# Performance work log

Measured on AMD Instinct MI355X. Metric: run time of the kernel, lower is better.

## Reference

```python
import jax, jax.numpy as jnp
import numpy as np

N, E, T = 4096, 49152, 262144
H, EMB, AIN, EB, TB = 256, 64, 92, 80, 40
NBLK = 12  # 4 alignn * 2 EGGC + 4 gcn


def _ln(x, s, b):
    mu = jnp.mean(x, -1, keepdims=True)
    v = jnp.mean((x - mu) ** 2, -1, keepdims=True)
    return (x - mu) * jax.lax.rsqrt(v + 1e-5) * s + b


def _mlp(x, W, b, s, bi):
    # Linear -> LayerNorm -> SiLU (MLPLayer)
    return jax.nn.silu(_ln(x @ W + b, s, bi))


def _rbf(x, vmin, vmax, bins):
    centers = jnp.linspace(vmin, vmax, bins)
    gamma = 1.0 / ((vmax - vmin) / (bins - 1))
    return jnp.exp(-gamma * (x[:, None] - centers) ** 2)


def _eggc(x, e, src, dst, W, b, ln_s, ln_b, n_nodes):
    # W: [5,H,H] = src_gate, dst_gate, edge_gate, src_update, dst_update
    m = (x @ W[0] + b[0])[src] + (x @ W[1] + b[1])[dst] + (e @ W[2] + b[2])
    sigma = jax.nn.sigmoid(m)
    sum_sh = jax.ops.segment_sum((x @ W[4] + b[4])[src] * sigma, dst, num_segments=n_nodes)
    sum_s = jax.ops.segment_sum(sigma, dst, num_segments=n_nodes)
    h = sum_sh / (sum_s + 1e-6)
    x_new = jax.nn.silu(_ln(x @ W[3] + b[3] + h, ln_s[0], ln_b[0]))
    e_new = jax.nn.silu(_ln(m, ln_s[1], ln_b[1]))
    return x + x_new, e + e_new  # residual=True


def setup_inputs() -> dict:
    key = jax.random.key(0)
    ks = jax.random.split(key, 16)
    s = 0.05
    return {
        "atom_features": jax.random.normal(ks[0], (N, AIN), jnp.float32),
        "r": jax.random.normal(ks[1], (E, 3), jnp.float32),
        "src": jax.random.randint(ks[2], (E,), 0, N),
        "dst": jax.random.randint(ks[3], (E,), 0, N),
        "lsrc": jax.random.randint(ks[4], (T,), 0, E),
        "ldst": jax.random.randint(ks[5], (T,), 0, E),
        "atom_W": s * jax.random.normal(ks[6], (AIN, H), jnp.float32),
        "atom_b": jnp.zeros((H,), jnp.float32),
        "atom_ln_s": jnp.ones((H,), jnp.float32),
        "atom_ln_b": jnp.zeros((H,), jnp.float32),
        "edge_W1": s * jax.random.normal(ks[7], (EB, EMB), jnp.float32),
        "edge_b1": jnp.zeros((EMB,), jnp.float32),
        "edge_ln1_s": jnp.ones((EMB,), jnp.float32),
        "edge_ln1_b": jnp.zeros((EMB,), jnp.float32),
        "edge_W2": s * jax.random.normal(ks[8], (EMB, H), jnp.float32),
        "edge_b2": jnp.zeros((H,), jnp.float32),
        "edge_ln2_s": jnp.ones((H,), jnp.float32),
        "edge_ln2_b": jnp.zeros((H,), jnp.float32),
        "ang_W1": s * jax.random.normal(ks[9], (TB, EMB), jnp.float32),
        "ang_b1": jnp.zeros((EMB,), jnp.float32),
        "ang_ln1_s": jnp.ones((EMB,), jnp.float32),
        "ang_ln1_b": jnp.zeros((EMB,), jnp.float32),
        "ang_W2": s * jax.random.normal(ks[10], (EMB, H), jnp.float32),
        "ang_b2": jnp.zeros((H,), jnp.float32),
        "ang_ln2_s": jnp.ones((H,), jnp.float32),
        "ang_ln2_b": jnp.zeros((H,), jnp.float32),
        "eggc_W": s * jax.random.normal(ks[11], (NBLK, 5, H, H), jnp.float32),
        "eggc_b": jnp.zeros((NBLK, 5, H), jnp.float32),
        "eggc_ln_s": jnp.ones((NBLK, 2, H), jnp.float32),
        "eggc_ln_b": jnp.zeros((NBLK, 2, H), jnp.float32),
        "fc_W": s * jax.random.normal(ks[12], (H, 1), jnp.float32),
        "fc_b": jnp.zeros((1,), jnp.float32),
    }


def reference(atom_features, r, src, dst, lsrc, ldst,
              atom_W, atom_b, atom_ln_s, atom_ln_b,
              edge_W1, edge_b1, edge_ln1_s, edge_ln1_b,
              edge_W2, edge_b2, edge_ln2_s, edge_ln2_b,
              ang_W1, ang_b1, ang_ln1_s, ang_ln1_b,
              ang_W2, ang_b2, ang_ln2_s, ang_ln2_b,
              eggc_W, eggc_b, eggc_ln_s, eggc_ln_b, fc_W, fc_b):
    # line-graph bond cosines: cos(-r_i, r_j) for each bond pair
    r1, r2 = -r[lsrc], r[ldst]
    cos = jnp.sum(r1 * r2, -1) / (jnp.linalg.norm(r1, axis=-1) * jnp.linalg.norm(r2, axis=-1))
    cos = jnp.clip(cos, -1.0, 1.0)
    z = _mlp(_mlp(_rbf(cos, -1.0, 1.0, TB), ang_W1, ang_b1, ang_ln1_s, ang_ln1_b),
             ang_W2, ang_b2, ang_ln2_s, ang_ln2_b)
    x = _mlp(atom_features, atom_W, atom_b, atom_ln_s, atom_ln_b)
    bondlength = jnp.linalg.norm(r, axis=1)
    y = _mlp(_mlp(_rbf(bondlength, 0.0, 8.0, EB), edge_W1, edge_b1, edge_ln1_s, edge_ln1_b),
             edge_W2, edge_b2, edge_ln2_s, edge_ln2_b)
    for i in range(4):  # alignn layers: crystal graph then line graph
        x, m = _eggc(x, y, src, dst, eggc_W[2 * i], eggc_b[2 * i], eggc_ln_s[2 * i], eggc_ln_b[2 * i], N)
        y, z = _eggc(m, z, lsrc, ldst, eggc_W[2 * i + 1], eggc_b[2 * i + 1], eggc_ln_s[2 * i + 1], eggc_ln_b[2 * i + 1], E)
    for i in range(4):  # gcn layers
        j = 8 + i
        x, y = _eggc(x, y, src, dst, eggc_W[j], eggc_b[j], eggc_ln_s[j], eggc_ln_b[j], N)
    atomwise_energy = x @ fc_W + fc_b  # [N,1]
    total_energy = jnp.mean(atomwise_energy)  # AvgPooling (eV/atom), single graph
    return total_energy, atomwise_energy
```

## Files before the change

### kernel.cpp

```cpp
#include <hip/hip_runtime.h>


typedef unsigned short bfu;
typedef __attribute__((ext_vector_type(8))) short short8;
typedef __attribute__((ext_vector_type(4))) float floatx4;

#define CHN 4096
#define CHCAP 24576
#define HH 65536

__device__ __forceinline__ float bf2f(bfu u) {
  union { unsigned u; float f; } x; x.u = ((unsigned)u) << 16; return x.f;
}
__device__ __forceinline__ bfu f2bf(float f) {
  union { float f; unsigned u; } x; x.f = f;
  unsigned r = x.u + 0x7FFFu + ((x.u >> 16) & 1u);
  return (bfu)(r >> 16);
}
__device__ __forceinline__ float fsig(float x) {
  return __builtin_amdgcn_rcpf(1.f + __expf(-x));
}
__device__ __forceinline__ float fsilu(float x) { return x * fsig(x); }

__device__ __forceinline__ void load_lds16(const bfu* g, bfu* l) {
  __builtin_amdgcn_global_load_lds(
      (const __attribute__((address_space(1))) void*)g,
      (__attribute__((address_space(3))) void*)l, 16, 0, 0);
}

struct f8 { float v[8]; };
__device__ __forceinline__ f8 ld8(const bfu* p) {
  short8 u = *(const short8*)(const void*)p;
  f8 r;
#pragma unroll
  for (int i = 0; i < 8; ++i) r.v[i] = bf2f((bfu)u[i]);
  return r;
}
__device__ __forceinline__ void st8(bfu* p, f8 x) {
  short8 u;
#pragma unroll
  for (int i = 0; i < 8; ++i) u[i] = (short)f2bf(x.v[i]);
  *(short8*)(void*)p = u;
}
__device__ __forceinline__ f8 add8(f8 a, f8 b) {
  f8 r;
#pragma unroll
  for (int i = 0; i < 8; ++i) r.v[i] = a.v[i] + b.v[i];
  return r;
}
__device__ __forceinline__ f8 sig8(f8 m) {
  f8 r;
#pragma unroll
  for (int i = 0; i < 8; ++i) r.v[i] = fsig(m.v[i]);
  return r;
}
__device__ __forceinline__ void wstats32(const f8& x, float& mean, float& rstd) {
  float s = 0.f, q = 0.f;
#pragma unroll
  for (int i = 0; i < 8; ++i) { s += x.v[i]; q += x.v[i] * x.v[i]; }
#pragma unroll
  for (int m = 1; m < 32; m <<= 1) { s += __shfl_xor(s, m); q += __shfl_xor(q, m); }
  mean = s * (1.f / 256.f);
  rstd = rsqrtf(fmaxf(q * (1.f / 256.f) - mean * mean, 0.f) + 1e-5f);
}
__device__ __forceinline__ f8 lnsilu8(f8 pre, f8 sg, f8 bb) {
  float mean, rstd; wstats32(pre, mean, rstd);
  f8 r;
#pragma unroll
  for (int i = 0; i < 8; ++i)
    r.v[i] = fsilu((pre.v[i] - mean) * rstd * sg.v[i] + bb.v[i]);
  return r;
}

__device__ __forceinline__ float block_sum256(float t, float* sm) {
#pragma unroll
  for (int o = 32; o; o >>= 1) t += __shfl_down(t, o);
  if ((threadIdx.x & 63) == 0) sm[threadIdx.x >> 6] = t;
  __syncthreads();
  float r = sm[0] + sm[1] + sm[2] + sm[3];
  __syncthreads();
  return r;
}

__global__ void probe_kernel(const unsigned* __restrict__ ones_raw, int* __restrict__ mode) {
  if (threadIdx.x == 0) *mode = (ones_raw[0] == 0x3F800000u) ? 1 : 0;
}
__global__ __launch_bounds__(256) void cvt_kernel(
    const void* __restrict__ src, bfu* __restrict__ dst, int n, const int* __restrict__ mode) {
  int i = blockIdx.x * 256 + threadIdx.x;
  if (i >= n) return;
  dst[i] = (*mode) ? f2bf(((const float*)src)[i]) : ((const bfu*)src)[i];
}
__global__ __launch_bounds__(256) void cvtf_kernel(
    const void* __restrict__ src, float* __restrict__ dst, int n, const int* __restrict__ mode) {
  int i = blockIdx.x * 256 + threadIdx.x;
  if (i >= n) return;
  dst[i] = (*mode) ? ((const float*)src)[i] : bf2f(((const bfu*)src)[i]);
}
struct CvtDesc { const void* src; bfu* dst; int n; };
struct CvtPack { CvtDesc e[20]; };
__global__ __launch_bounds__(256) void cvt_batch_kernel(CvtPack p, const int* __restrict__ mode) {
  CvtDesc d = p.e[blockIdx.y];
  int i = blockIdx.x * 256 + threadIdx.x;
  if (i >= d.n) return;
  d.dst[i] = (*mode) ? f2bf(((const float*)d.src)[i]) : ((const bfu*)d.src)[i];
}

template<int BM, int BN, int WR, int WC>
__device__ __forceinline__ void gemm_body(
    const bfu* __restrict__ A, const bfu* __restrict__ Bt,
    const bfu* __restrict__ bias, bfu* __restrict__ Cout,
    int cnt, int N, int K, int base, int m0, int n0)
{
  constexpr int WM = BM / WR, WN = BN / WC;
  constexpr int TM = WM / 16, TN = WN / 16;
  static __shared__ __align__(16) bfu As[BM * 64];
  static __shared__ __align__(16) bfu Bs[BN * 64];

  const int tid = threadIdx.x, wave = tid >> 6, lane = tid & 63;
  const int wr = wave / WC, wc = wave % WC;
  const int lrow = lane & 15, kq = (lane >> 4) * 8;

  floatx4 acc[TM][TN];
#pragma unroll
  for (int i = 0; i < TM; ++i)
#pragma unroll
    for (int j = 0; j < TN; ++j) acc[i][j] = (floatx4){0.f, 0.f, 0.f, 0.f};

  for (int k0 = 0; k0 < K; k0 += 64) {
#pragma unroll
    for (int it = 0; it < BM / 32; ++it) {
      int ch = it * 256 + tid;
      int row = ch >> 3, kc = (ch & 7) << 3;
      int r = m0 + row;
      int ar = base + (r < cnt ? r : cnt - 1);
      load_lds16(A + (size_t)ar * K + k0 + kc, As + (size_t)(it * 256 + wave * 64) * 8);
    }
#pragma unroll
    for (int it = 0; it < BN / 32; ++it) {
      int ch = it * 256 + tid;
      int row = ch >> 3, kc = (ch & 7) << 3;
      load_lds16(Bt + (size_t)(n0 + row) * K + k0 + kc, Bs + (size_t)(it * 256 + wave * 64) * 8);
    }
    __syncthreads();
#pragma unroll
    for (int s = 0; s < 2; ++s) {
      short8 Af[TM], Bf[TN];
#pragma unroll
      for (int i = 0; i < TM; ++i)
        Af[i] = *(const short8*)(const void*)(As + (wr * WM + i * 16 + lrow) * 64 + s * 32 + kq);
#pragma unroll
      for (int j = 0; j < TN; ++j)
        Bf[j] = *(const short8*)(const void*)(Bs + (wc * WN + j * 16 + lrow) * 64 + s * 32 + kq);
#pragma unroll
      for (int i = 0; i < TM; ++i)
#pragma unroll
        for (int j = 0; j < TN; ++j)
          acc[i][j] = __builtin_amdgcn_mfma_f32_16x16x32_bf16(Af[i], Bf[j], acc[i][j], 0, 0, 0);
    }
    __syncthreads();
  }

  const int rquad = lane >> 4, cin = lane & 15;
#pragma unroll
  for (int i = 0; i < TM; ++i) {
#pragma unroll
    for (int rr = 0; rr < 4; ++rr) {
      int orow = m0 + wr * WM + i * 16 + rquad * 4 + rr;
      if (orow >= cnt) continue;
#pragma unroll
      for (int j = 0; j < TN; ++j) {
        int gcol = n0 + wc * WN + j * 16 + cin;
        Cout[(size_t)orow * N + gcol] = f2bf(acc[i][j][rr] + bf2f(bias[gcol]));
      }
    }
  }
}

template<int BM, int BN, int WR, int WC>
__global__ __launch_bounds__(256) void gemm_kernel(
    const bfu* __restrict__ A, const bfu* __restrict__ Bt,
    const bfu* __restrict__ bias, bfu* __restrict__ Cout, int M, int N, int K)
{
  gemm_body<BM, BN, WR, WC>(A, Bt, bias, Cout, M, N, K, 0,
                            blockIdx.x * BM, blockIdx.y * BN);
}

__global__ __launch_bounds__(256) void line_gemm_kernel(
    const bfu* __restrict__ z, const bfu* __restrict__ yb,
    const bfu* __restrict__ W, const bfu* __restrict__ bb,
    bfu* __restrict__ mchunk, bfu* __restrict__ u3c,
    const int* __restrict__ loff, int n0, int n1)
{
  if (blockIdx.y < 2) {
    int base = loff[n0], cnt = loff[n1] - base;
    int m0 = blockIdx.x * 128;
    if (m0 >= cnt) return;
    gemm_body<128, 128, 2, 2>(z, W + 4 * HH, bb + 4 * 256, mchunk,
                              cnt, 256, 256, base, m0, blockIdx.y * 128);
  } else {
    if (blockIdx.x >= 64) return;
    gemm_body<128, 128, 2, 2>(yb + (size_t)n0 * 256, W + 3 * HH, bb + 3 * 256, u3c,
                              CHN, 256, 256, 0, (blockIdx.x & 31) * 128, (blockIdx.x >> 5) * 128);
  }
}

__global__ __launch_bounds__(256) void atom_gemm_kernel(
    const bfu* __restrict__ x, const bfu* __restrict__ y,
    const bfu* __restrict__ W, const bfu* __restrict__ bb,
    bfu* __restrict__ afused, bfu* __restrict__ mbufa)
{
  if (blockIdx.x < 384) {
    gemm_body<128, 128, 2, 2>(y, W + 4 * HH, bb + 4 * 256, mbufa,
                              49152, 256, 256, 0, blockIdx.x * 128, blockIdx.y * 128);
  } else {
    int lid = (blockIdx.x - 384) * 2 + blockIdx.y;
    gemm_body<128, 128, 2, 2>(x, W, bb, afused,
                              4096, 1024, 256, 0, (lid >> 3) * 128, (lid & 7) * 128);
  }
}

__global__ __launch_bounds__(256) void line_gates_kernel(
    const bfu* __restrict__ y, const bfu* __restrict__ z,
    const bfu* __restrict__ W, const bfu* __restrict__ bb,
    bfu* __restrict__ lfused, bfu* __restrict__ mch0, bfu* __restrict__ u3c0,
    const int* __restrict__ loff)
{
  if (blockIdx.y < 6) {
    gemm_body<128, 128, 2, 2>(y, W, bb, lfused,
                              49152, 768, 256, 0, blockIdx.x * 128, blockIdx.y * 128);
  } else if (blockIdx.y < 8) {
    int cnt = loff[CHN];
    int m0 = blockIdx.x * 128;
    if (blockIdx.x >= CHCAP / 128 || m0 >= cnt) return;
    gemm_body<128, 128, 2, 2>(z, W + 4 * HH, bb + 4 * 256, mch0,
                              cnt, 256, 256, 0, m0, (blockIdx.y - 6) * 128);
  } else {
    if (blockIdx.x >= 64) return;
    gemm_body<128, 128, 2, 2>(y, W + 3 * HH, bb + 3 * 256, u3c0,
                              CHN, 256, 256, 0, (blockIdx.x & 31) * 128, (blockIdx.x >> 5) * 128);
  }
}

__global__ __launch_bounds__(256) void cosbl_kernel(
    const float* __restrict__ r, const int* __restrict__ lsrc_p,
    const int* __restrict__ ldst_p, float* __restrict__ cosv,
    float* __restrict__ bl, int T, int E)
{
  int idx = blockIdx.x * 256 + threadIdx.x;
  if (idx < T) {
    int e1 = lsrc_p[idx], e2 = ldst_p[idx];
    float ax = -r[e1 * 3 + 0], ay = -r[e1 * 3 + 1], az = -r[e1 * 3 + 2];
    float bx =  r[e2 * 3 + 0], by =  r[e2 * 3 + 1], bz =  r[e2 * 3 + 2];
    float dot = ax * bx + ay * by + az * bz;
    float na = sqrtf(ax * ax + ay * ay + az * az);
    float nb = sqrtf(bx * bx + by * by + bz * bz);
    float c = dot / (na * nb);
    cosv[idx] = fminf(1.f, fmaxf(-1.f, c));
  } else if (idx < T + E) {
    int e = idx - T;
    float x = r[e * 3 + 0], yv = r[e * 3 + 1], zv = r[e * 3 + 2];
    bl[e] = sqrtf(x * x + yv * yv + zv * zv);
  }
}

template<int KP, int BINS, int IS_ANG>
__global__ __launch_bounds__(256) void mlp1_ln_kernel(
    const float* __restrict__ v, const bfu* __restrict__ Bt,
    const bfu* __restrict__ bias, const bfu* __restrict__ lns,
    const bfu* __restrict__ lnb, bfu* __restrict__ outp, int M)
{
  constexpr int LDT = KP + 8;
  __shared__ bfu As[128 * LDT];
  const int tid = threadIdx.x, wave = tid >> 6, lane = tid & 63;
  const int lrow = lane & 15, kq = (lane >> 4) * 8;
  const int m0 = blockIdx.x * 128;

  for (int idx = tid; idx < 128 * (KP / 8); idx += 256) {
    int row = idx / (KP / 8), kc = (idx % (KP / 8)) * 8;
    float val = v[m0 + row];
    short8 pack;
#pragma unroll
    for (int jj = 0; jj < 8; ++jj) {
      int k = kc + jj;
      float e = 0.f;
      if (k < BINS) {
        float center = IS_ANG ? (-1.f + k * (2.f / 39.f)) : (k * (8.f / 79.f));
        float d = val - center;
        e = __expf((IS_ANG ? -19.5f : -9.875f) * d * d);
      }
      pack[jj] = (short)f2bf(e);
    }
    *(short8*)(void*)(As + row * LDT + kc) = pack;
  }
  __syncthreads();

  floatx4 acc[2][4];
#pragma unroll
  for (int i = 0; i < 2; ++i)
#pragma unroll
    for (int j = 0; j < 4; ++j) acc[i][j] = (floatx4){0.f, 0.f, 0.f, 0.f};
#pragma unroll
  for (int ks = 0; ks < KP / 32; ++ks) {
    short8 Af[2], Bf[4];
#pragma unroll
    for (int j = 0; j < 4; ++j)
      Bf[j] = *(const short8*)(const void*)(Bt + (size_t)(j * 16 + lrow) * KP + ks * 32 + kq);
#pragma unroll
    for (int i = 0; i < 2; ++i)
      Af[i] = *(const short8*)(const void*)(As + (wave * 32 + i * 16 + lrow) * LDT + ks * 32 + kq);
#pragma unroll
    for (int i = 0; i < 2; ++i)
#pragma unroll
      for (int j = 0; j < 4; ++j)
        acc[i][j] = __builtin_amdgcn_mfma_f32_16x16x32_bf16(Af[i], Bf[j], acc[i][j], 0, 0, 0);
  }

  const int rquad = lane >> 4, cin = lane & 15;
  float bj[4], sj[4], lj[4];
#pragma unroll
  for (int j = 0; j < 4; ++j) {
    bj[j] = bf2f(bias[j * 16 + cin]);
    sj[j] = bf2f(lns[j * 16 + cin]);
    lj[j] = bf2f(lnb[j * 16 + cin]);
  }
#pragma unroll
  for (int i = 0; i < 2; ++i) {
#pragma unroll
    for (int rr = 0; rr < 4; ++rr) {
      int row = m0 + wave * 32 + i * 16 + rquad * 4 + rr;
      float pre[4], s = 0.f, q = 0.f;
#pragma unroll
      for (int j = 0; j < 4; ++j) {
        pre[j] = acc[i][j][rr] + bj[j];
        s += pre[j]; q += pre[j] * pre[j];
      }
#pragma unroll
      for (int mm = 1; mm < 16; mm <<= 1) { s += __shfl_xor(s, mm); q += __shfl_xor(q, mm); }
      float mean = s * (1.f / 64.f);
      float rstd = rsqrtf(fmaxf(q * (1.f / 64.f) - mean * mean, 0.f) + 1e-5f);
#pragma unroll
      for (int j = 0; j < 4; ++j) {
        float u = (pre[j] - mean) * rstd * sj[j] + lj[j];
        outp[(size_t)row * 64 + j * 16 + cin] = f2bf(fsilu(u));
      }
    }
  }
}

__global__ __launch_bounds__(256) void mlp2_ln_kernel(
    const bfu* __restrict__ A, const bfu* __restrict__ Bt,
    const bfu* __restrict__ bias, const bfu* __restrict__ lns,
    const bfu* __restrict__ lnb, bfu* __restrict__ outp, int M)
{
  __shared__ float part[64 * 8];
  const int tid = threadIdx.x, wave = tid >> 6, lane = tid & 63;
  const int lrow = lane & 15, kq = (lane >> 4) * 8;
  const int m0 = blockIdx.x * 64;

  short8 Bf[2][4];
#pragma unroll
  for (int s = 0; s < 2; ++s)
#pragma unroll
    for (int j = 0; j < 4; ++j)
      Bf[s][j] = *(const short8*)(const void*)(
          Bt + (size_t)(wave * 64 + j * 16 + lrow) * 64 + s * 32 + kq);

  floatx4 acc[4][4];
#pragma unroll
  for (int i = 0; i < 4; ++i)
#pragma unroll
    for (int j = 0; j < 4; ++j) acc[i][j] = (floatx4){0.f, 0.f, 0.f, 0.f};
#pragma unroll
  for (int s = 0; s < 2; ++s) {
    short8 Af[4];
#pragma unroll
    for (int i = 0; i < 4; ++i)
      Af[i] = *(const short8*)(const void*)(
          A + (size_t)(m0 + i * 16 + lrow) * 64 + s * 32 + kq);
#pragma unroll
    for (int i = 0; i < 4; ++i)
#pragma unroll
      for (int j = 0; j < 4; ++j)
        acc[i][j] = __builtin_amdgcn_mfma_f32_16x16x32_bf16(Af[i], Bf[s][j], acc[i][j], 0, 0, 0);
  }

  const int rquad = lane >> 4, cin = lane & 15;
  float bj[4], sj[4], lj[4];
#pragma unroll
  for (int j = 0; j < 4; ++j) {
    int col = wave * 64 + j * 16 + cin;
    bj[j] = bf2f(bias[col]); sj[j] = bf2f(lns[col]); lj[j] = bf2f(lnb[col]);
  }
#pragma unroll
  for (int i = 0; i < 4; ++i) {
#pragma unroll
    for (int rr = 0; rr < 4; ++rr) {
      float s = 0.f, q = 0.f;
#pragma unroll
      for (int j = 0; j < 4; ++j) {
        float p = acc[i][j][rr] + bj[j];
        s += p; q += p * p;
      }
#pragma unroll
      for (int mm = 1; mm < 16; mm <<= 1) { s += __shfl_xor(s, mm); q += __shfl_xor(q, mm); }
      if (cin == 0) {
        int row = i * 16 + rquad * 4 + rr;
        part[row * 8 + wave * 2] = s;
        part[row * 8 + wave * 2 + 1] = q;
      }
    }
  }
  __syncthreads();
#pragma unroll
  for (int i = 0; i < 4; ++i) {
#pragma unroll
    for (int rr = 0; rr < 4; ++rr) {
      int row = i * 16 + rquad * 4 + rr;
      float s = part[row * 8] + part[row * 8 + 2] + part[row * 8 + 4] + part[row * 8 + 6];
      float q = part[row * 8 + 1] + part[row * 8 + 3] + part[row * 8 + 5] + part[row * 8 + 7];
      float mean = s * (1.f / 256.f);
      float rstd = rsqrtf(fmaxf(q * (1.f / 256.f) - mean * mean, 0.f) + 1e-5f);
#pragma unroll
      for (int j = 0; j < 4; ++j) {
        float u = (acc[i][j][rr] + bj[j] - mean) * rstd * sj[j] + lj[j];
        outp[(size_t)(m0 + row) * 256 + wave * 64 + j * 16 + cin] = f2bf(fsilu(u));
      }
    }
  }
}

__global__ __launch_bounds__(256) void count_kernel(
    const int* __restrict__ d, int* __restrict__ cnt, int ne) {
  int i = blockIdx.x * 256 + threadIdx.x;
  if (i < ne) atomicAdd(&cnt[d[i]], 1);
}
__global__ __launch_bounds__(256) void scan_kernel(
    const int* __restrict__ cnt, int* __restrict__ off, int n) {
  __shared__ int ssum[256];
  __shared__ int sbase[257];
  int t = threadIdx.x;
  int strip = (n + 255) / 256;
  int lo = t * strip, hi = lo + strip; if (hi > n) hi = n; if (lo > n) lo = n;
  int s = 0;
  for (int i = lo; i < hi; ++i) s += cnt[i];
  ssum[t] = s;
  __syncthreads();
  if (t == 0) {
    int run = 0;
    for (int i = 0; i < 256; ++i) { sbase[i] = run; run += ssum[i]; }
    sbase[256] = run;
  }
  __syncthreads();
  int run = sbase[t];
  for (int i = lo; i < hi; ++i) { off[i] = run; run += cnt[i]; }
  if (t == 0) off[n] = sbase[256];
}
__global__ __launch_bounds__(256) void copy_kernel(
    const int* __restrict__ a, int* __restrict__ b, int n) {
  int i = blockIdx.x * 256 + threadIdx.x;
  if (i < n) b[i] = a[i];
}
__global__ __launch_bounds__(256) void fill_kernel(
    const int* __restrict__ d, int* __restrict__ cur, int* __restrict__ ids, int ne) {
  int i = blockIdx.x * 256 + threadIdx.x;
  if (i < ne) ids[atomicAdd(&cur[d[i]], 1)] = i;
}
__global__ __launch_bounds__(256) void fill2_kernel(
    const int* __restrict__ ldst, const int* __restrict__ lsrc, int* __restrict__ cur,
    int* __restrict__ lsrc_p, int* __restrict__ ldst_p, int ne) {
  int i = blockIdx.x * 256 + threadIdx.x;
  if (i >= ne) return;
  int d = ldst[i];
  int pos = atomicAdd(&cur[d], 1);
  lsrc_p[pos] = lsrc[i];
  ldst_p[pos] = d;
}

__global__ __launch_bounds__(256) void transpose_pad_kernel(
    const void* __restrict__ W, bfu* __restrict__ Wt, int K, int N, int Kp,
    const int* __restrict__ mode)
{
  int idx = blockIdx.x * 256 + threadIdx.x;
  if (idx >= N * Kp) return;
  int n = idx / Kp, k = idx - n * Kp;
  bfu v = 0;
  if (k < K) {
    size_t si = (size_t)k * N + n;
    v = (*mode) ? f2bf(((const float*)W)[si]) : ((const bfu*)W)[si];
  }
  Wt[idx] = v;
}
__device__ __forceinline__ int slot2mat(int slot) {
  const int m[5] = {0, 4, 1, 3, 2};
  return m[slot];
}
__global__ __launch_bounds__(256) void transpose_eggc_kernel(
    const void* __restrict__ W, bfu* __restrict__ Wt, const int* __restrict__ mode)
{
  int bs = blockIdx.y;
  int blk = bs / 5, slot = bs - blk * 5;
  int mat = slot2mat(slot);
  int idx = blockIdx.x * 256 + threadIdx.x;
  int n = idx >> 8, k = idx & 255;
  size_t si = ((size_t)(blk * 5 + mat) * 256 + k) * 256 + n;
  bfu v = (*mode) ? f2bf(((const float*)W)[si]) : ((const bfu*)W)[si];
  Wt[((size_t)bs * 256 + n) * 256 + k] = v;
}
__global__ __launch_bounds__(256) void bias_perm_kernel(
    const void* __restrict__ B, bfu* __restrict__ Bp, const int* __restrict__ mode)
{
  int i = blockIdx.x * 256 + threadIdx.x;
  int bs = i >> 8, c = i & 255;
  int blk = bs / 5, slot = bs - blk * 5;
  int mat = slot2mat(slot);
  size_t si = (size_t)(blk * 5 + mat) * 256 + c;
  Bp[i] = (*mode) ? f2bf(((const float*)B)[si]) : ((const bfu*)B)[si];
}

__global__ __launch_bounds__(256) void atom_fused_kernel(
    const bfu* __restrict__ mbuf, const bfu* __restrict__ af,
    const int* __restrict__ src,
    bfu* __restrict__ X, bfu* __restrict__ Y,
    const int* __restrict__ aoff, const int* __restrict__ aids,
    int do_edge,
    const bfu* __restrict__ lns, const bfu* __restrict__ lnb,
    const bfu* __restrict__ les, const bfu* __restrict__ leb)
{
  int wave = threadIdx.x >> 6, lane = threadIdx.x & 63;
  int half = lane >> 5, c8 = (lane & 31) * 8;
  int n = blockIdx.x * 4 + wave;
  int p0 = aoff[n], p1 = aoff[n + 1];
  f8 g1 = ld8(af + (size_t)n * 1024 + 512 + c8);
  f8 esg = {}, ebb = {};
  if (do_edge) { esg = ld8(les + c8); ebb = ld8(leb + c8); }
  f8 num = {}, den = {};
  for (int p = p0 + half; p < p1; p += 2) {
    int id = aids[p], sx = src[id];
    f8 m = add8(add8(ld8(mbuf + (size_t)id * 256 + c8),
                     ld8(af + (size_t)sx * 1024 + c8)), g1);
    f8 sg = sig8(m);
    f8 u4 = ld8(af + (size_t)sx * 1024 + 256 + c8);
#pragma unroll
    for (int i = 0; i < 8; ++i) {
      num.v[i] += sg.v[i] * u4.v[i];
      den.v[i] += sg.v[i];
    }
    if (do_edge) {
      f8 sil = lnsilu8(m, esg, ebb);
      bfu* op = Y + (size_t)id * 256 + c8;
      st8(op, add8(sil, ld8(op)));
    }
  }
#pragma unroll
  for (int i = 0; i < 8; ++i) {
    num.v[i] += __shfl_xor(num.v[i], 32);
    den.v[i] += __shfl_xor(den.v[i], 32);
  }
  f8 u3 = ld8(af + (size_t)n * 1024 + 768 + c8);
  f8 pre;
#pragma unroll
  for (int i = 0; i < 8; ++i)
    pre.v[i] = u3.v[i] + num.v[i] / (den.v[i] + 1e-6f);
  f8 sil = lnsilu8(pre, ld8(lns + c8), ld8(lnb + c8));
  if (half == 0) {
    bfu* op = X + (size_t)n * 256 + c8;
    st8(op, add8(sil, ld8(op)));
  }
}

__global__ __launch_bounds__(256) void line_fused_kernel(
    const bfu* __restrict__ mchunk, const bfu* __restrict__ lf,
    const bfu* __restrict__ u3c,
    const int* __restrict__ loff, const int* __restrict__ lsrc_p,
    bfu* __restrict__ Z, bfu* __restrict__ Y,
    int n0, int do_edge,
    const bfu* __restrict__ lns, const bfu* __restrict__ lnb,
    const bfu* __restrict__ les, const bfu* __restrict__ leb)
{
  int wave = threadIdx.x >> 6, lane = threadIdx.x & 63;
  int half = lane >> 5, c8 = (lane & 31) * 8;
  int n = n0 + blockIdx.x * 4 + wave;
  int p0 = loff[n], p1 = loff[n + 1], base = loff[n0];
  f8 g1 = ld8(lf + (size_t)n * 768 + 512 + c8);
  f8 esg = {}, ebb = {};
  if (do_edge) { esg = ld8(les + c8); ebb = ld8(leb + c8); }
  f8 num = {}, den = {};
  for (int p = p0 + half; p < p1; p += 2) {
    int sx = lsrc_p[p];
    f8 m = add8(add8(ld8(mchunk + (size_t)(p - base) * 256 + c8),
                     ld8(lf + (size_t)sx * 768 + c8)), g1);
    f8 sg = sig8(m);
    f8 u4 = ld8(lf + (size_t)sx * 768 + 256 + c8);
#pragma unroll
    for (int i = 0; i < 8; ++i) {
      num.v[i] += sg.v[i] * u4.v[i];
      den.v[i] += sg.v[i];
    }
    if (do_edge) {
      f8 sil = lnsilu8(m, esg, ebb);
      bfu* op = Z + (size_t)p * 256 + c8;
      st8(op, add8(sil, ld8(op)));
    }
  }
#pragma unroll
  for (int i = 0; i < 8; ++i) {
    num.v[i] += __shfl_xor(num.v[i], 32);
    den.v[i] += __shfl_xor(den.v[i], 32);
  }
  f8 u3 = ld8(u3c + (size_t)(n - n0) * 256 + c8);
  f8 pre;
#pragma unroll
  for (int i = 0; i < 8; ++i)
    pre.v[i] = u3.v[i] + num.v[i] / (den.v[i] + 1e-6f);
  f8 sil = lnsilu8(pre, ld8(lns + c8), ld8(lnb + c8));
  if (half == 0) {
    bfu* op = Y + (size_t)n * 256 + c8;
    st8(op, add8(sil, ld8(op)));
  }
}

__global__ __launch_bounds__(256) void atom_init_kernel(
    const bfu* __restrict__ af, const bfu* __restrict__ W, const bfu* __restrict__ bias,
    const bfu* __restrict__ lns, const bfu* __restrict__ lnb, bfu* __restrict__ X)
{
  __shared__ float sm[4];
  int row = blockIdx.x, c = threadIdx.x;
  float acc = bf2f(bias[c]);
  for (int k = 0; k < 92; ++k)
    acc += bf2f(af[row * 92 + k]) * bf2f(W[k * 256 + c]);
  float mean = block_sum256(acc, sm) * (1.f / 256.f);
  float d = acc - mean;
  float var = block_sum256(d * d, sm) * (1.f / 256.f);
  float u = d * rsqrtf(var + 1e-5f) * bf2f(lns[c]) + bf2f(lnb[c]);
  X[(size_t)row * 256 + c] = f2bf(fsilu(u));
}

__global__ __launch_bounds__(256) void final_kernel(
    const bfu* __restrict__ X, const bfu* __restrict__ fcW, const bfu* __restrict__ fcb,
    void* __restrict__ out, float* __restrict__ acc, const int* __restrict__ mode)
{
  int row = blockIdx.x * 4 + (threadIdx.x >> 6);
  int lane = threadIdx.x & 63;
  float s = 0.f;
#pragma unroll
  for (int k = 0; k < 4; ++k)
    s += bf2f(X[(size_t)row * 256 + lane + k * 64]) * bf2f(fcW[lane + k * 64]);
#pragma unroll
  for (int o = 32; o; o >>= 1) s += __shfl_down(s, o);
  if (lane == 0) {
    float v = s + bf2f(fcb[0]);
    if (*mode) ((float*)out)[1 + row] = v;
    else       ((bfu*)out)[1 + row] = f2bf(v);
    atomicAdd(acc, v);
  }
}
__global__ void mean_kernel(const float* __restrict__ acc, void* __restrict__ out,
                            const int* __restrict__ mode) {
  if (threadIdx.x == 0) {
    float v = acc[0] * (1.f / 4096.f);
    if (*mode) ((float*)out)[0] = v;
    else       ((bfu*)out)[0] = f2bf(v);
  }
}
__global__ void dbg_kernel(void* __restrict__ out, float v) {
  if (threadIdx.x == 0) { ((bfu*)out)[0] = f2bf(v); }
}

extern "C" void kernel_launch(void* const* d_in, const int* in_sizes, int n_in,
                              void* d_out, int out_size, void* d_ws, size_t ws_size,
                              hipStream_t stream) {
  const int N = 4096, E = 49152, T = 262144, H = 256;

  const int* src  = (const int*)d_in[2];
  const int* dst  = (const int*)d_in[3];
  const int* lsrc = (const int*)d_in[4];
  const int* ldst = (const int*)d_in[5];

  char* bp = (char*)d_ws;
  size_t off = 0;
  auto carve = [&](size_t bytes) -> char* {
    char* q = bp + off;
    off = (off + bytes + 255) & ~(size_t)255;
    return q;
  };
  bfu* x       = (bfu*)carve((size_t)N * H * 2);
  bfu* y       = (bfu*)carve((size_t)E * H * 2);
  bfu* z       = (bfu*)carve((size_t)T * H * 2);
  bfu* reg     = (bfu*)carve((size_t)E * 768 * 2);
  bfu* u3c     = (bfu*)carve((size_t)CHN * H * 2);
  bfu* mchunk  = (bfu*)carve((size_t)CHCAP * H * 2);
  bfu* WtE     = (bfu*)carve((size_t)60 * H * H * 2);
  bfu* ebp     = (bfu*)carve((size_t)12 * 5 * H * 2);
  bfu* Wt_a1   = (bfu*)carve(64 * 64 * 2);
  bfu* Wt_a2   = (bfu*)carve(256 * 64 * 2);
  bfu* Wt_e1   = (bfu*)carve(64 * 128 * 2);
  bfu* Wt_e2   = (bfu*)carve(256 * 64 * 2);
  int* aoff    = (int*)carve((size_t)(N + 1) * 4);
  int* aids    = (int*)carve((size_t)E * 4);
  int* loff    = (int*)carve((size_t)(E + 1) * 4);
  int* lsrc_p  = (int*)carve((size_t)T * 4);
  int* ldst_p  = (int*)carve((size_t)T * 4);
  int* cursors = (int*)carve((size_t)E * 4);
  float* macc  = (float*)carve(256);
  int* mode    = (int*)carve(256);
  bfu* par_c   = (bfu*)carve(8192 * 2);
  bfu* els_c   = (bfu*)carve((size_t)12 * 2 * H * 2);
  bfu* elb_c   = (bfu*)carve((size_t)12 * 2 * H * 2);

  if (off > ws_size) {
    hipMemsetAsync(d_out, 0, (size_t)out_size * 2, stream);
    dbg_kernel<<<1, 64, 0, stream>>>(d_out, (float)(ws_size >> 20));
    return;
  }

  char* tail = (char*)reg + (size_t)52 * 1024 * 1024;
  bfu* af_c  = (bfu*)tail;                 tail += ((size_t)N * 92 * 2 + 255) & ~255ull;
  float* r_f = (float*)tail;               tail += ((size_t)E * 3 * 4 + 255) & ~255ull;
  float* cosv = (float*)tail;              tail += ((size_t)T * 4 + 255) & ~255ull;
  float* blv = (float*)tail;               tail += ((size_t)E * 4 + 255) & ~255ull;
  bfu* atW_c = (bfu*)tail;

  bfu* atom_b_c   = par_c + 0;
  bfu* atom_lns_c = par_c + 256;
  bfu* atom_lnb_c = par_c + 512;
  bfu* e_b1_c     = par_c + 768;
  bfu* e_l1s_c    = par_c + 832;
  bfu* e_l1b_c    = par_c + 896;
  bfu* e_b2_c     = par_c + 1024;
  bfu* e_l2s_c    = par_c + 1280;
  bfu* e_l2b_c    = par_c + 1536;
  bfu* a_b1_c     = par_c + 1792;
  bfu* a_l1s_c    = par_c + 1856;
  bfu* a_l1b_c    = par_c + 1920;
  bfu* a_b2_c     = par_c + 2048;
  bfu* a_l2s_c    = par_c + 2304;
  bfu* a_l2b_c    = par_c + 2560;
  bfu* fcW_c      = par_c + 2816;
  bfu* fcb_c      = par_c + 3072;

  bfu* lfused = reg;
  bfu* afused = reg;
  bfu* mbufa  = reg + (size_t)N * 1024;
  bfu* emb_t  = reg;
  bfu* emb_e  = reg + (size_t)T * 64;

  probe_kernel<<<1, 64, 0, stream>>>((const unsigned*)d_in[8], mode);
  CvtPack pk;
  int ii = 0;
  auto add = [&](int idx, bfu* dstp, int n) { pk.e[ii++] = {d_in[idx], dstp, n}; };
  add(7, atom_b_c, 256);  add(8, atom_lns_c, 256); add(9, atom_lnb_c, 256);
  add(11, e_b1_c, 64);    add(12, e_l1s_c, 64);    add(13, e_l1b_c, 64);
  add(15, e_b2_c, 256);   add(16, e_l2s_c, 256);   add(17, e_l2b_c, 256);
  add(19, a_b1_c, 64);    add(20, a_l1s_c, 64);    add(21, a_l1b_c, 64);
  add(23, a_b2_c, 256);   add(24, a_l2s_c, 256);   add(25, a_l2b_c, 256);
  add(30, fcW_c, 256);    add(31, fcb_c, 1);
  add(28, els_c, 12 * 2 * 256);
  add(29, elb_c, 12 * 2 * 256);
  add(6, atW_c, 92 * 256);
  cvt_batch_kernel<<<dim3(92, 20), 256, 0, stream>>>(pk, mode);
  cvt_kernel<<<(N * 92 + 255) / 256, 256, 0, stream>>>(d_in[0], af_c, N * 92, mode);
  cvtf_kernel<<<(E * 3 + 255) / 256, 256, 0, stream>>>(d_in[1], r_f, E * 3, mode);

  hipMemsetAsync(cursors, 0, (size_t)N * 4, stream);
  count_kernel<<<E / 256, 256, 0, stream>>>(dst, cursors, E);
  scan_kernel<<<1, 256, 0, stream>>>(cursors, aoff, N);
  copy_kernel<<<(N + 255) / 256, 256, 0, stream>>>(aoff, cursors, N);
  fill_kernel<<<E / 256, 256, 0, stream>>>(dst, cursors, aids, E);

  hipMemsetAsync(cursors, 0, (size_t)E * 4, stream);
  count_kernel<<<T / 256, 256, 0, stream>>>(ldst, cursors, T);
  scan_kernel<<<1, 256, 0, stream>>>(cursors, loff, E);
  copy_kernel<<<(E + 255) / 256, 256, 0, stream>>>(loff, cursors, E);
  fill2_kernel<<<T / 256, 256, 0, stream>>>(ldst, lsrc, cursors, lsrc_p, ldst_p, T);

  transpose_eggc_kernel<<<dim3(256, 60), 256, 0, stream>>>(d_in[26], WtE, mode);
  bias_perm_kernel<<<60, 256, 0, stream>>>(d_in[27], ebp, mode);
  transpose_pad_kernel<<<16, 256, 0, stream>>>(d_in[18], Wt_a1, 40, 64, 64, mode);
  transpose_pad_kernel<<<64, 256, 0, stream>>>(d_in[22], Wt_a2, 64, 256, 64, mode);
  transpose_pad_kernel<<<32, 256, 0, stream>>>(d_in[10], Wt_e1, 80, 64, 128, mode);
  transpose_pad_kernel<<<64, 256, 0, stream>>>(d_in[14], Wt_e2, 64, 256, 64, mode);

  cosbl_kernel<<<(T + E + 255) / 256, 256, 0, stream>>>(r_f, lsrc_p, ldst_p, cosv, blv, T, E);
  mlp1_ln_kernel<64, 40, 1><<<T / 128, 256, 0, stream>>>(
      cosv, Wt_a1, a_b1_c, a_l1s_c, a_l1b_c, emb_t, T);
  mlp2_ln_kernel<<<T / 64, 256, 0, stream>>>(emb_t, Wt_a2, a_b2_c, a_l2s_c, a_l2b_c, z, T);
  mlp1_ln_kernel<128, 80, 0><<<E / 128, 256, 0, stream>>>(
      blv, Wt_e1, e_b1_c, e_l1s_c, e_l1b_c, emb_e, E);
  mlp2_ln_kernel<<<E / 64, 256, 0, stream>>>(emb_e, Wt_e2, e_b2_c, e_l2s_c, e_l2b_c, y, E);

  atom_init_kernel<<<N, 256, 0, stream>>>(af_c, atW_c, atom_b_c, atom_lns_c, atom_lnb_c, x);

  auto atom_eggc = [&](int blk, int do_edge) {
    const bfu* W  = WtE + (size_t)blk * 5 * HH;
    const bfu* bb = ebp + (size_t)blk * 5 * H;
    const bfu* ls = els_c + (size_t)blk * 2 * H;
    const bfu* lb = elb_c + (size_t)blk * 2 * H;
    atom_gemm_kernel<<<dim3(512, 2), 256, 0, stream>>>(x, y, W, bb, afused, mbufa);
    atom_fused_kernel<<<N / 4, 256, 0, stream>>>(
        mbufa, afused, src, x, y, aoff, aids, do_edge, ls, lb, ls + H, lb + H);
  };

  auto line_eggc = [&](int blk, int do_edge) {
    const bfu* W  = WtE + (size_t)blk * 5 * HH;
    const bfu* bb = ebp + (size_t)blk * 5 * H;
    const bfu* ls = els_c + (size_t)blk * 2 * H;
    const bfu* lb = elb_c + (size_t)blk * 2 * H;
    line_gates_kernel<<<dim3(384, 9), 256, 0, stream>>>(
        y, z, W, bb, lfused, mchunk, u3c, loff);
    for (int c = 0; c < E / CHN; ++c) {
      int n0 = c * CHN;
      line_fused_kernel<<<CHN / 4, 256, 0, stream>>>(
          mchunk, lfused, u3c, loff, lsrc_p, z, y, n0, do_edge,
          ls, lb, ls + H, lb + H);
      if (c + 1 < E / CHN)
        line_gemm_kernel<<<dim3(CHCAP / 128, 3), 256, 0, stream>>>(
            z, y, W, bb, mchunk, u3c, loff, n0 + CHN, n0 + 2 * CHN);
    }
  };

  for (int i = 0; i < 4; ++i) {
    atom_eggc(2 * i, 1);
    line_eggc(2 * i + 1, i < 3);
  }
  for (int i = 0; i < 4; ++i)
    atom_eggc(8 + i, i < 3);

  hipMemsetAsync(macc, 0, 4, stream);
  final_kernel<<<N / 4, 256, 0, stream>>>(x, fcW_c, fcb_c, d_out, macc, mode);
  mean_kernel<<<1, 64, 0, stream>>>(macc, d_out, mode);
}
```

Before: 2.564 ms.

## Fuse two-layer embedding MLPs into one kernel and compute cosines during line-graph fill

```diff
diff --git a/kernel.cpp b/kernel.cpp
--- a/kernel.cpp
+++ b/kernel.cpp
@@ -242,41 +242,34 @@
   }
 }
 
-__global__ __launch_bounds__(256) void cosbl_kernel(
-    const float* __restrict__ r, const int* __restrict__ lsrc_p,
-    const int* __restrict__ ldst_p, float* __restrict__ cosv,
-    float* __restrict__ bl, int T, int E)
-{
-  int idx = blockIdx.x * 256 + threadIdx.x;
-  if (idx < T) {
-    int e1 = lsrc_p[idx], e2 = ldst_p[idx];
-    float ax = -r[e1 * 3 + 0], ay = -r[e1 * 3 + 1], az = -r[e1 * 3 + 2];
-    float bx =  r[e2 * 3 + 0], by =  r[e2 * 3 + 1], bz =  r[e2 * 3 + 2];
-    float dot = ax * bx + ay * by + az * bz;
-    float na = sqrtf(ax * ax + ay * ay + az * az);
-    float nb = sqrtf(bx * bx + by * by + bz * bz);
-    float c = dot / (na * nb);
-    cosv[idx] = fminf(1.f, fmaxf(-1.f, c));
-  } else if (idx < T + E) {
-    int e = idx - T;
-    float x = r[e * 3 + 0], yv = r[e * 3 + 1], zv = r[e * 3 + 2];
-    bl[e] = sqrtf(x * x + yv * yv + zv * zv);
-  }
+__global__ __launch_bounds__(256) void bl_kernel(
+    const float* __restrict__ r, float* __restrict__ bl, int E)
+{
+  int e = blockIdx.x * 256 + threadIdx.x;
+  if (e >= E) return;
+  float x = r[e * 3 + 0], yv = r[e * 3 + 1], zv = r[e * 3 + 2];
+  bl[e] = sqrtf(x * x + yv * yv + zv * zv);
 }
 
 template<int KP, int BINS, int IS_ANG>
-__global__ __launch_bounds__(256) void mlp1_ln_kernel(
-    const float* __restrict__ v, const bfu* __restrict__ Bt,
-    const bfu* __restrict__ bias, const bfu* __restrict__ lns,
-    const bfu* __restrict__ lnb, bfu* __restrict__ outp, int M)
+__global__ __launch_bounds__(256) void mlp_fused_kernel(
+    const float* __restrict__ v,
+    const bfu* __restrict__ B1t, const bfu* __restrict__ b1,
+    const bfu* __restrict__ l1s, const bfu* __restrict__ l1b,
+    const bfu* __restrict__ B2t, const bfu* __restrict__ b2,
+    const bfu* __restrict__ l2s, const bfu* __restrict__ l2b,
+    bfu* __restrict__ outp)
 {
   constexpr int LDT = KP + 8;
-  __shared__ bfu As[128 * LDT];
+  __shared__ bfu As[64 * LDT];
+  __shared__ bfu Em[64 * 72];
+  __shared__ float part[64 * 8];
   const int tid = threadIdx.x, wave = tid >> 6, lane = tid & 63;
   const int lrow = lane & 15, kq = (lane >> 4) * 8;
-  const int m0 = blockIdx.x * 128;
-
-  for (int idx = tid; idx < 128 * (KP / 8); idx += 256) {
+  const int rquad = lane >> 4, cin = lane & 15;
+  const int m0 = blockIdx.x * 64;
+
+  for (int idx = tid; idx < 64 * (KP / 8); idx += 256) {
     int row = idx / (KP / 8), kc = (idx % (KP / 8)) * 8;
     float val = v[m0 + row];
     short8 pack;
@@ -295,44 +288,33 @@
   }
   __syncthreads();
 
-  floatx4 acc[2][4];
-#pragma unroll
-  for (int i = 0; i < 2; ++i)
-#pragma unroll
-    for (int j = 0; j < 4; ++j) acc[i][j] = (floatx4){0.f, 0.f, 0.f, 0.f};
+  floatx4 a1[4];
+#pragma unroll
+  for (int j = 0; j < 4; ++j) a1[j] = (floatx4){0.f, 0.f, 0.f, 0.f};
 #pragma unroll
   for (int ks = 0; ks < KP / 32; ++ks) {
-    short8 Af[2], Bf[4];
-#pragma unroll
-    for (int j = 0; j < 4; ++j)
-      Bf[j] = *(const short8*)(const void*)(Bt + (size_t)(j * 16 + lrow) * KP + ks * 32 + kq);
-#pragma unroll
-    for (int i = 0; i < 2; ++i)
-      Af[i] = *(const short8*)(const void*)(As + (wave * 32 + i * 16 + lrow) * LDT + ks * 32 + kq);
-#pragma unroll
-    for (int i = 0; i < 2; ++i)
-#pragma unroll
-      for (int j = 0; j < 4; ++j)
-        acc[i][j] = __builtin_amdgcn_mfma_f32_16x16x32_bf16(Af[i], Bf[j], acc[i][j], 0, 0, 0);
-  }
-
-  const int rquad = lane >> 4, cin = lane & 15;
-  float bj[4], sj[4], lj[4];
-#pragma unroll
-  for (int j = 0; j < 4; ++j) {
-    bj[j] = bf2f(bias[j * 16 + cin]);
-    sj[j] = bf2f(lns[j * 16 + cin]);
-    lj[j] = bf2f(lnb[j * 16 + cin]);
-  }
-#pragma unroll
-  for (int i = 0; i < 2; ++i) {
+    short8 Af = *(const short8*)(const void*)(As + (wave * 16 + lrow) * LDT + ks * 32 + kq);
+#pragma unroll
+    for (int j = 0; j < 4; ++j) {
+      short8 Bf = *(const short8*)(const void*)(B1t + (size_t)(j * 16 + lrow) * KP + ks * 32 + kq);
+      a1[j] = __builtin_amdgcn_mfma_f32_16x16x32_bf16(Af, Bf, a1[j], 0, 0, 0);
+    }
+  }
+  {
+    float bj[4], sj[4], lj[4];
+#pragma unroll
+    for (int j = 0; j < 4; ++j) {
+      bj[j] = bf2f(b1[j * 16 + cin]);
+      sj[j] = bf2f(l1s[j * 16 + cin]);
+      lj[j] = bf2f(l1b[j * 16 + cin]);
+    }
 #pragma unroll
     for (int rr = 0; rr < 4; ++rr) {
-      int row = m0 + wave * 32 + i * 16 + rquad * 4 + rr;
+      int rl = wave * 16 + rquad * 4 + rr;
       float pre[4], s = 0.f, q = 0.f;
 #pragma unroll
       for (int j = 0; j < 4; ++j) {
-        pre[j] = acc[i][j][rr] + bj[j];
+        pre[j] = a1[j][rr] + bj[j];
         s += pre[j]; q += pre[j] * pre[j];
       }
 #pragma unroll
@@ -342,29 +324,19 @@
 #pragma unroll
       for (int j = 0; j < 4; ++j) {
         float u = (pre[j] - mean) * rstd * sj[j] + lj[j];
-        outp[(size_t)row * 64 + j * 16 + cin] = f2bf(fsilu(u));
+        Em[rl * 72 + j * 16 + cin] = f2bf(fsilu(u));
       }
     }
   }
-}
-
-__global__ __launch_bounds__(256) void mlp2_ln_kernel(
-    const bfu* __restrict__ A, const bfu* __restrict__ Bt,
-    const bfu* __restrict__ bias, const bfu* __restrict__ lns,
-    const bfu* __restrict__ lnb, bfu* __restrict__ outp, int M)
-{
-  __shared__ float part[64 * 8];
-  const int tid = threadIdx.x, wave = tid >> 6, lane = tid & 63;
-  const int lrow = lane & 15, kq = (lane >> 4) * 8;
-  const int m0 = blockIdx.x * 64;
-
-  short8 Bf[2][4];
+  __syncthreads();
+
+  short8 Bf2[2][4];
 #pragma unroll
   for (int s = 0; s < 2; ++s)
 #pragma unroll
     for (int j = 0; j < 4; ++j)
-      Bf[s][j] = *(const short8*)(const void*)(
-          Bt + (size_t)(wave * 64 + j * 16 + lrow) * 64 + s * 32 + kq);
+      Bf2[s][j] = *(const short8*)(const void*)(
+          B2t + (size_t)(wave * 64 + j * 16 + lrow) * 64 + s * 32 + kq);
 
   floatx4 acc[4][4];
 #pragma unroll
@@ -376,21 +348,19 @@
     short8 Af[4];
 #pragma unroll
     for (int i = 0; i < 4; ++i)
-      Af[i] = *(const short8*)(const void*)(
-          A + (size_t)(m0 + i * 16 + lrow) * 64 + s * 32 + kq);
+      Af[i] = *(const short8*)(const void*)(Em + (i * 16 + lrow) * 72 + s * 32 + kq);
 #pragma unroll
     for (int i = 0; i < 4; ++i)
 #pragma unroll
       for (int j = 0; j < 4; ++j)
-        acc[i][j] = __builtin_amdgcn_mfma_f32_16x16x32_bf16(Af[i], Bf[s][j], acc[i][j], 0, 0, 0);
-  }
-
-  const int rquad = lane >> 4, cin = lane & 15;
+        acc[i][j] = __builtin_amdgcn_mfma_f32_16x16x32_bf16(Af[i], Bf2[s][j], acc[i][j], 0, 0, 0);
+  }
+
   float bj[4], sj[4], lj[4];
 #pragma unroll
   for (int j = 0; j < 4; ++j) {
     int col = wave * 64 + j * 16 + cin;
-    bj[j] = bf2f(bias[col]); sj[j] = bf2f(lns[col]); lj[j] = bf2f(lnb[col]);
+    bj[j] = bf2f(b2[col]); sj[j] = bf2f(l2s[col]); lj[j] = bf2f(l2b[col]);
   }
 #pragma unroll
   for (int i = 0; i < 4; ++i) {
@@ -468,13 +438,20 @@
 }
 __global__ __launch_bounds__(256) void fill2_kernel(
     const int* __restrict__ ldst, const int* __restrict__ lsrc, int* __restrict__ cur,
-    int* __restrict__ lsrc_p, int* __restrict__ ldst_p, int ne) {
+    int* __restrict__ lsrc_p, float* __restrict__ cosv,
+    const float* __restrict__ r, int ne) {
   int i = blockIdx.x * 256 + threadIdx.x;
   if (i >= ne) return;
-  int d = ldst[i];
+  int d = ldst[i], e1 = lsrc[i];
   int pos = atomicAdd(&cur[d], 1);
-  lsrc_p[pos] = lsrc[i];
-  ldst_p[pos] = d;
+  lsrc_p[pos] = e1;
+  float ax = -r[e1 * 3 + 0], ay = -r[e1 * 3 + 1], az = -r[e1 * 3 + 2];
+  float bx =  r[d * 3 + 0],  by =  r[d * 3 + 1],  bz =  r[d * 3 + 2];
+  float dot = ax * bx + ay * by + az * bz;
+  float na = sqrtf(ax * ax + ay * ay + az * az);
+  float nb = sqrtf(bx * bx + by * by + bz * bz);
+  float c = dot / (na * nb);
+  cosv[pos] = fminf(1.f, fmaxf(-1.f, c));
 }
 
 __global__ __launch_bounds__(256) void transpose_pad_kernel(
@@ -700,7 +677,6 @@
   int* aids    = (int*)carve((size_t)E * 4);
   int* loff    = (int*)carve((size_t)(E + 1) * 4);
   int* lsrc_p  = (int*)carve((size_t)T * 4);
-  int* ldst_p  = (int*)carve((size_t)T * 4);
   int* cursors = (int*)carve((size_t)E * 4);
   float* macc  = (float*)carve(256);
   int* mode    = (int*)carve(256);
@@ -742,8 +718,6 @@
   bfu* lfused = reg;
   bfu* afused = reg;
   bfu* mbufa  = reg + (size_t)N * 1024;
-  bfu* emb_t  = reg;
-  bfu* emb_e  = reg + (size_t)T * 64;
 
   probe_kernel<<<1, 64, 0, stream>>>((const unsigned*)d_in[8], mode);
   CvtPack pk;
@@ -772,7 +746,7 @@
   count_kernel<<<T / 256, 256, 0, stream>>>(ldst, cursors, T);
   scan_kernel<<<1, 256, 0, stream>>>(cursors, loff, E);
   copy_kernel<<<(E + 255) / 256, 256, 0, stream>>>(loff, cursors, E);
-  fill2_kernel<<<T / 256, 256, 0, stream>>>(ldst, lsrc, cursors, lsrc_p, ldst_p, T);
+  fill2_kernel<<<T / 256, 256, 0, stream>>>(ldst, lsrc, cursors, lsrc_p, cosv, r_f, T);
 
   transpose_eggc_kernel<<<dim3(256, 60), 256, 0, stream>>>(d_in[26], WtE, mode);
   bias_perm_kernel<<<60, 256, 0, stream>>>(d_in[27], ebp, mode);
@@ -781,13 +755,11 @@
   transpose_pad_kernel<<<32, 256, 0, stream>>>(d_in[10], Wt_e1, 80, 64, 128, mode);
   transpose_pad_kernel<<<64, 256, 0, stream>>>(d_in[14], Wt_e2, 64, 256, 64, mode);
 
-  cosbl_kernel<<<(T + E + 255) / 256, 256, 0, stream>>>(r_f, lsrc_p, ldst_p, cosv, blv, T, E);
-  mlp1_ln_kernel<64, 40, 1><<<T / 128, 256, 0, stream>>>(
-      cosv, Wt_a1, a_b1_c, a_l1s_c, a_l1b_c, emb_t, T);
-  mlp2_ln_kernel<<<T / 64, 256, 0, stream>>>(emb_t, Wt_a2, a_b2_c, a_l2s_c, a_l2b_c, z, T);
-  mlp1_ln_kernel<128, 80, 0><<<E / 128, 256, 0, stream>>>(
-      blv, Wt_e1, e_b1_c, e_l1s_c, e_l1b_c, emb_e, E);
-  mlp2_ln_kernel<<<E / 64, 256, 0, stream>>>(emb_e, Wt_e2, e_b2_c, e_l2s_c, e_l2b_c, y, E);
+  bl_kernel<<<(E + 255) / 256, 256, 0, stream>>>(r_f, blv, E);
+  mlp_fused_kernel<64, 40, 1><<<T / 64, 256, 0, stream>>>(
+      cosv, Wt_a1, a_b1_c, a_l1s_c, a_l1b_c, Wt_a2, a_b2_c, a_l2s_c, a_l2b_c, z);
+  mlp_fused_kernel<128, 80, 0><<<E / 64, 256, 0, stream>>>(
+      blv, Wt_e1, e_b1_c, e_l1s_c, e_l1b_c, Wt_e2, e_b2_c, e_l2s_c, e_l2b_c, y);
 
   atom_init_kernel<<<N, 256, 0, stream>>>(af_c, atW_c, atom_b_c, atom_lns_c, atom_lnb_c, x);
 
```

Measured after the change: 2.703 ms. +5.4%, slower.
